# Kernel tuning notes

Measured on AMD Instinct MI355X. Metric: run time of the kernel, lower is better.

The kernel has to match this reference:

```python
import jax, jax.numpy as jnp
import numpy as np

VAL = 1.0  # shift weight value

def shift_plus(x, val=VAL):
    """Per-channel-group spatial shift ('+' mode), equivalent to the
    groups=C 3x3 conv with a single nonzero tap per channel, padding=1.
    x: [B, C, H, W], C % 5 == 0.
    """
    c = x.shape[1]
    cgp = c // 5
    xp = jnp.pad(x, ((0, 0), (0, 0), (1, 1), (1, 1)))
    g0 = xp[:, 0 * cgp:1 * cgp, 1:-1, 2:]    # tap (1,2): pull from w+1
    g1 = xp[:, 1 * cgp:2 * cgp, 1:-1, :-2]   # tap (1,0): pull from w-1
    g2 = xp[:, 2 * cgp:3 * cgp, 2:, 1:-1]    # tap (2,1): pull from h+1
    g3 = xp[:, 3 * cgp:4 * cgp, :-2, 1:-1]   # tap (0,1): pull from h-1
    g4 = x[:, 4 * cgp:, :, :]                # tap (1,1): identity
    return jnp.concatenate([g0, g1, g2, g3, g4], axis=1) * val

def shift_conv1x1(x, w, b):
    # shift then pointwise conv (1x1) with bias
    xs = shift_plus(x)
    y = jnp.einsum('bchw,oc->bohw', xs, w)
    return y + b[None, :, None, None]

def setup_inputs() -> dict:
    key = jax.random.key(0)
    k1, k2, k3, k4, k5 = jax.random.split(key, 5)
    B, Cin, H, W = 8, 100, 256, 256
    Chid, Cout = 200, 100
    x = jax.random.normal(k1, (B, Cin, H, W), dtype=jnp.float32)
    w1 = jax.random.normal(k2, (Chid, Cin), dtype=jnp.float32) * 0.02
    b1 = jax.random.normal(k3, (Chid,), dtype=jnp.float32) * 0.02
    w2 = jax.random.normal(k4, (Cout, Chid), dtype=jnp.float32) * 0.02
    b2 = jax.random.normal(k5, (Cout,), dtype=jnp.float32) * 0.02
    return {"x": x, "w1": w1, "b1": b1, "w2": w2, "b2": b2}

def reference(x, w1, b1, w2, b2):
    h = shift_conv1x1(x, w1, b1)
    h = jax.nn.gelu(h, approximate=False)  # torch nn.GELU default is exact erf
    return shift_conv1x1(h, w2, b2)
```

## Files before the change

### kernel.cpp

```cpp
#include <hip/hip_runtime.h>
#include <math.h>

typedef unsigned short u16;
typedef unsigned int   u32;
typedef short bf16x8 __attribute__((ext_vector_type(8)));
typedef float f32x4  __attribute__((ext_vector_type(4)));

__device__ __forceinline__ u16 f2bf(float f) {
  u32 u = __builtin_bit_cast(u32, f);
  u32 r = (u + 0x7fffu + ((u >> 16) & 1u)) >> 16;
  return (u16)r;
}
__device__ __forceinline__ float gelu_exact(float v) {
  return 0.5f * v * (1.0f + erff(v * 0.70710678118654752f));
}

#define H_BYTES   209715200ll
#define FW1_ELEMS 26624
#define FW2_ELEMS 25088

__global__ void prep_frags(const float* __restrict__ w1, const float* __restrict__ w2,
                           u16* __restrict__ fw1, u16* __restrict__ fw2) {
  int gid = blockIdx.x * 256 + threadIdx.x;
  if (gid < FW1_ELEMS) {
    int j = gid & 7, lane = (gid >> 3) & 63, rest = gid >> 9;
    int nt = rest % 13, kc = rest / 13;
    int c = kc * 32 + (lane >> 4) * 8 + j;
    int o = nt * 16 + (lane & 15);
    float v = (c < 100 && o < 200) ? w1[o * 100 + c] : 0.f;
    fw1[gid] = f2bf(v);
  } else if (gid < FW1_ELEMS + FW2_ELEMS) {
    int i2 = gid - FW1_ELEMS;
    int j = i2 & 7, lane = (i2 >> 3) & 63, rest = i2 >> 9;
    int nt = rest % 7, kc = rest / 7;
    int c = kc * 32 + (lane >> 4) * 8 + j;
    int o = nt * 16 + (lane & 15);
    float v = (c < 200 && o < 100) ? w2[o * 200 + c] : 0.f;
    fw2[i2] = f2bf(v);
  }
}

#define SK1  136
#define SKO1 208
__global__ __launch_bounds__(256, 3) void conv1_kernel(
    const float* __restrict__ x, const u16* __restrict__ fw1,
    const float* __restrict__ b1, u16* __restrict__ hbuf) {
  __shared__ __align__(16) char smem[128 * SKO1 * 2];
  u16* At = (u16*)smem;
  u16* Ot = (u16*)smem;
  const int t   = threadIdx.x;
  const int bid = blockIdx.x;
  const int bx  = ((bid & 7) << 9) | (bid >> 3);
  const int r  = bx >> 1;
  const int b  = r >> 8;
  const int hh = r & 255;
  const int w0 = (bx & 1) << 7;

  {
    const int m  = t & 127;
    const int kh = t >> 7;
    const int wp = w0 + m;
    #pragma unroll
    for (int g = 0; g < 8; ++g) {
      const int c0 = 8 * (kh + 2 * g);
      u32 pk[4];
      #pragma unroll
      for (int jj = 0; jj < 8; ++jj) {
        const int c = c0 + jj;
        float v = 0.f;
        if (c < 100) {
          const int dw = (c < 20) ? 1 : ((c < 40) ? -1 : 0);
          const int dh = (c >= 40 && c < 60) ? 1 : ((c >= 60 && c < 80) ? -1 : 0);
          const int hs = hh + dh, ws = wp + dw;
          if ((unsigned)hs < 256u && (unsigned)ws < 256u)
            v = x[((b * 100 + c) * 256 + hs) * 256 + ws];
        }
        const u32 bv = f2bf(v);
        if (jj & 1) pk[jj >> 1] |= bv << 16; else pk[jj >> 1] = bv;
      }
      *(uint4*)&At[m * SK1 + c0] = make_uint4(pk[0], pk[1], pk[2], pk[3]);
    }
  }
  __syncthreads();

  const int lane = t & 63, wid = t >> 6;
  const int col = lane & 15, q = lane >> 4;
  f32x4 acc[2][13];
  #pragma unroll
  for (int i = 0; i < 2; ++i)
    #pragma unroll
    for (int nt = 0; nt < 13; ++nt) acc[i][nt] = (f32x4)0.0f;

  const bf16x8* wf = (const bf16x8*)fw1 + lane;
  #pragma unroll 1
  for (int kc = 0; kc < 4; ++kc) {
    const bf16x8 a0 = *(const bf16x8*)&At[((2 * wid + 0) * 16 + col) * SK1 + kc * 32 + q * 8];
    const bf16x8 a1 = *(const bf16x8*)&At[((2 * wid + 1) * 16 + col) * SK1 + kc * 32 + q * 8];
    #pragma unroll
    for (int nt = 0; nt < 13; ++nt) {
      const bf16x8 bf = wf[(kc * 13 + nt) * 64];
      acc[0][nt] = __builtin_amdgcn_mfma_f32_16x16x32_bf16(bf, a0, acc[0][nt], 0, 0, 0);
      acc[1][nt] = __builtin_amdgcn_mfma_f32_16x16x32_bf16(bf, a1, acc[1][nt], 0, 0, 0);
    }
  }

  __syncthreads();

  #pragma unroll
  for (int nt = 0; nt < 13; ++nt) {
    const int ob = nt * 16 + 4 * q;
    const float4 bias4 = (ob <= 196) ? *(const float4*)&b1[ob]
                                     : make_float4(0.f, 0.f, 0.f, 0.f);
    #pragma unroll
    for (int i = 0; i < 2; ++i) {
      const f32x4 v = acc[i][nt];
      const int px = (2 * wid + i) * 16 + col;
      const u32 p0 = (u32)f2bf(gelu_exact(v[0] + bias4.x)) |
                     ((u32)f2bf(gelu_exact(v[1] + bias4.y)) << 16);
      const u32 p1 = (u32)f2bf(gelu_exact(v[2] + bias4.z)) |
                     ((u32)f2bf(gelu_exact(v[3] + bias4.w)) << 16);
      *(uint2*)&Ot[px * SKO1 + ob] = make_uint2(p0, p1);
    }
  }
  __syncthreads();
  {
    const int rowbase = ((b * 256 + hh) * 256 + w0) * 200;
    #pragma unroll
    for (int s = 0; s < 13; ++s) {
      const int id = s * 256 + t;
      if (id < 3200) {
        const int px = id / 25;
        const int ch = id - px * 25;
        const uint4 d = *(const uint4*)&Ot[px * SKO1 + ch * 8];
        *(uint4*)&hbuf[rowbase + px * 200 + ch * 8] = d;
      }
    }
  }
}

#define SK2 232
#define PS2 132
__global__ __launch_bounds__(256, 2) void conv2_kernel(
    const u16* __restrict__ hbuf, const u16* __restrict__ fw2,
    const float* __restrict__ b2, float* __restrict__ out) {
  __shared__ __align__(16) char smem[128 * SK2 * 2];
  u16*   At = (u16*)smem;
  float* Ob = (float*)smem;
  const int t   = threadIdx.x;
  const int bid = blockIdx.x;
  const int bx  = ((bid & 7) << 9) | (bid >> 3);
  const int r  = bx >> 1;
  const int b  = r >> 8;
  const int hh = r & 255;
  const int w0 = (bx & 1) << 7;

  {
    const int m  = t & 127;
    const int kh = t >> 7;
    const int wp = w0 + m;
    if (kh == 0) {
      const uint4 z = make_uint4(0u, 0u, 0u, 0u);
      *(uint4*)&At[m * SK2 + 200] = z;
      *(uint4*)&At[m * SK2 + 208] = z;
      *(uint4*)&At[m * SK2 + 216] = z;
    }
    #pragma unroll
    for (int g = 0; g < 13; ++g) {
      const int c0 = 8 * (kh + 2 * g);
      if (c0 < 200) {
        const int dw = (c0 < 40) ? 1 : ((c0 < 80) ? -1 : 0);
        const int dh = (c0 >= 80 && c0 < 120) ? 1 : ((c0 >= 120 && c0 < 160) ? -1 : 0);
        const int hs = hh + dh, ws = wp + dw;
        const bool ok = ((unsigned)hs < 256u) && ((unsigned)ws < 256u);
        const int hsc = ok ? hs : hh;
        const int wsc = ok ? ws : wp;
        uint4 d = *(const uint4*)&hbuf[((b * 256 + hsc) * 256 + wsc) * 200 + c0];
        if (!ok) d = make_uint4(0u, 0u, 0u, 0u);
        *(uint4*)&At[m * SK2 + c0] = d;
      }
    }
  }
  __syncthreads();

  const int lane = t & 63, wid = t >> 6;
  const int col = lane & 15, q = lane >> 4;
  f32x4 acc[2][7];
  #pragma unroll
  for (int i = 0; i < 2; ++i)
    #pragma unroll
    for (int nt = 0; nt < 7; ++nt) acc[i][nt] = (f32x4)0.0f;

  const bf16x8* wf = (const bf16x8*)fw2 + lane;
  #pragma unroll 1
  for (int kc = 0; kc < 7; ++kc) {
    const bf16x8 a0 = *(const bf16x8*)&At[((2 * wid + 0) * 16 + col) * SK2 + kc * 32 + q * 8];
    const bf16x8 a1 = *(const bf16x8*)&At[((2 * wid + 1) * 16 + col) * SK2 + kc * 32 + q * 8];
    #pragma unroll
    for (int nt = 0; nt < 7; ++nt) {
      const bf16x8 bf = wf[(kc * 7 + nt) * 64];
      acc[0][nt] = __builtin_amdgcn_mfma_f32_16x16x32_bf16(a0, bf, acc[0][nt], 0, 0, 0);
      acc[1][nt] = __builtin_amdgcn_mfma_f32_16x16x32_bf16(a1, bf, acc[1][nt], 0, 0, 0);
    }
  }

  __syncthreads();

  #pragma unroll
  for (int nt = 0; nt < 7; ++nt) {
    const int o = nt * 16 + col;
    const float bias = (o < 100) ? b2[o] : 0.f;
    #pragma unroll
    for (int i = 0; i < 2; ++i) {
      const f32x4 v = acc[i][nt];
      *(float4*)&Ob[o * PS2 + (2 * wid + i) * 16 + 4 * q] =
          make_float4(v[0] + bias, v[1] + bias, v[2] + bias, v[3] + bias);
    }
  }
  __syncthreads();
  {
    const int obase = (b * 100 * 256 + hh) * 256 + w0;
    #pragma unroll
    for (int s = 0; s < 13; ++s) {
      const int id = s * 256 + t;
      if (id < 3200) {
        const int oo = id >> 5, ch = id & 31;
        const float4 d = *(const float4*)&Ob[oo * PS2 + ch * 4];
        *(float4*)&out[obase + oo * 65536 + ch * 4] = d;
      }
    }
  }
}

extern "C" void kernel_launch(void* const* d_in, const int* in_sizes, int n_in,
                              void* d_out, int out_size, void* d_ws, size_t ws_size,
                              hipStream_t stream) {
  const float* x  = (const float*)d_in[0];
  const float* w1 = (const float*)d_in[1];
  const float* b1 = (const float*)d_in[2];
  const float* w2 = (const float*)d_in[3];
  const float* b2 = (const float*)d_in[4];
  float* out = (float*)d_out;

  u16* hbuf = (u16*)d_ws;
  u16* fw1  = (u16*)((char*)d_ws + H_BYTES);
  u16* fw2  = (u16*)((char*)d_ws + H_BYTES + FW1_ELEMS * 2);

  prep_frags<<<202, 256, 0, stream>>>(w1, w2, fw1, fw2);
  conv1_kernel<<<4096, 256, 0, stream>>>(x, fw1, b1, hbuf);
  conv2_kernel<<<4096, 256, 0, stream>>>(hbuf, fw2, b2, out);
}
```

Before: 608.2 us.

## Halve pixel tile per block to 64 and raise occupancy in both conv kernels

Both conv kernels now process 64 pixels per block instead of 128, and the grid doubles to 8192 blocks. Each wave handles one 16-pixel M-tile, which halves the accumulator registers and shared memory per block, and launch bounds rise to 4 blocks per SM. The goal is more waves in flight to hide global-memory latency in these bandwidth-bound kernels. In exchange, each weight fragment loaded from global or cache is reused across fewer pixels, and the row writes from each block become shorter.

```diff
diff --git a/kernel.cpp b/kernel.cpp
--- a/kernel.cpp
+++ b/kernel.cpp
@@ -42,27 +42,30 @@
 
 #define SK1  136
 #define SKO1 208
-__global__ __launch_bounds__(256, 3) void conv1_kernel(
+__global__ __launch_bounds__(256, 4) void conv1_kernel(
     const float* __restrict__ x, const u16* __restrict__ fw1,
     const float* __restrict__ b1, u16* __restrict__ hbuf) {
-  __shared__ __align__(16) char smem[128 * SKO1 * 2];
+  __shared__ __align__(16) char smem[64 * SKO1 * 2];
   u16* At = (u16*)smem;
   u16* Ot = (u16*)smem;
   const int t   = threadIdx.x;
   const int bid = blockIdx.x;
-  const int bx  = ((bid & 7) << 9) | (bid >> 3);
-  const int r  = bx >> 1;
-  const int b  = r >> 8;
-  const int hh = r & 255;
-  const int w0 = (bx & 1) << 7;
-
-  {
-    const int m  = t & 127;
-    const int kh = t >> 7;
+  const int bx  = ((bid & 7) << 10) | (bid >> 3);
+  const int b  = bx >> 10;
+  const int hh = (bx >> 2) & 255;
+  const int w0 = (bx & 3) << 6;
+
+  {
+    const int m  = t & 63;
+    const int kh = t >> 6;
     const int wp = w0 + m;
     #pragma unroll
-    for (int g = 0; g < 8; ++g) {
-      const int c0 = 8 * (kh + 2 * g);
+    for (int g = 0; g < 4; ++g) {
+      const int c0 = 8 * (kh + 4 * g);
+      if (c0 >= 100) {
+        *(uint4*)&At[m * SK1 + c0] = make_uint4(0u, 0u, 0u, 0u);
+        continue;
+      }
       u32 pk[4];
       #pragma unroll
       for (int jj = 0; jj < 8; ++jj) {
@@ -85,22 +88,18 @@
 
   const int lane = t & 63, wid = t >> 6;
   const int col = lane & 15, q = lane >> 4;
-  f32x4 acc[2][13];
-  #pragma unroll
-  for (int i = 0; i < 2; ++i)
-    #pragma unroll
-    for (int nt = 0; nt < 13; ++nt) acc[i][nt] = (f32x4)0.0f;
+  f32x4 acc[13];
+  #pragma unroll
+  for (int nt = 0; nt < 13; ++nt) acc[nt] = (f32x4)0.0f;
 
   const bf16x8* wf = (const bf16x8*)fw1 + lane;
   #pragma unroll 1
   for (int kc = 0; kc < 4; ++kc) {
-    const bf16x8 a0 = *(const bf16x8*)&At[((2 * wid + 0) * 16 + col) * SK1 + kc * 32 + q * 8];
-    const bf16x8 a1 = *(const bf16x8*)&At[((2 * wid + 1) * 16 + col) * SK1 + kc * 32 + q * 8];
+    const bf16x8 a = *(const bf16x8*)&At[(wid * 16 + col) * SK1 + kc * 32 + q * 8];
     #pragma unroll
     for (int nt = 0; nt < 13; ++nt) {
       const bf16x8 bf = wf[(kc * 13 + nt) * 64];
-      acc[0][nt] = __builtin_amdgcn_mfma_f32_16x16x32_bf16(bf, a0, acc[0][nt], 0, 0, 0);
-      acc[1][nt] = __builtin_amdgcn_mfma_f32_16x16x32_bf16(bf, a1, acc[1][nt], 0, 0, 0);
+      acc[nt] = __builtin_amdgcn_mfma_f32_16x16x32_bf16(bf, a, acc[nt], 0, 0, 0);
     }
   }
 
@@ -111,24 +110,21 @@
     const int ob = nt * 16 + 4 * q;
     const float4 bias4 = (ob <= 196) ? *(const float4*)&b1[ob]
                                      : make_float4(0.f, 0.f, 0.f, 0.f);
-    #pragma unroll
-    for (int i = 0; i < 2; ++i) {
-      const f32x4 v = acc[i][nt];
-      const int px = (2 * wid + i) * 16 + col;
-      const u32 p0 = (u32)f2bf(gelu_exact(v[0] + bias4.x)) |
-                     ((u32)f2bf(gelu_exact(v[1] + bias4.y)) << 16);
-      const u32 p1 = (u32)f2bf(gelu_exact(v[2] + bias4.z)) |
-                     ((u32)f2bf(gelu_exact(v[3] + bias4.w)) << 16);
-      *(uint2*)&Ot[px * SKO1 + ob] = make_uint2(p0, p1);
-    }
+    const f32x4 v = acc[nt];
+    const int px = wid * 16 + col;
+    const u32 p0 = (u32)f2bf(gelu_exact(v[0] + bias4.x)) |
+                   ((u32)f2bf(gelu_exact(v[1] + bias4.y)) << 16);
+    const u32 p1 = (u32)f2bf(gelu_exact(v[2] + bias4.z)) |
+                   ((u32)f2bf(gelu_exact(v[3] + bias4.w)) << 16);
+    *(uint2*)&Ot[px * SKO1 + ob] = make_uint2(p0, p1);
   }
   __syncthreads();
   {
     const int rowbase = ((b * 256 + hh) * 256 + w0) * 200;
     #pragma unroll
-    for (int s = 0; s < 13; ++s) {
+    for (int s = 0; s < 7; ++s) {
       const int id = s * 256 + t;
-      if (id < 3200) {
+      if (id < 1600) {
         const int px = id / 25;
         const int ch = id - px * 25;
         const uint4 d = *(const uint4*)&Ot[px * SKO1 + ch * 8];
@@ -139,67 +135,58 @@
 }
 
 #define SK2 232
-#define PS2 132
-__global__ __launch_bounds__(256, 2) void conv2_kernel(
+#define PS2 68
+__global__ __launch_bounds__(256, 4) void conv2_kernel(
     const u16* __restrict__ hbuf, const u16* __restrict__ fw2,
     const float* __restrict__ b2, float* __restrict__ out) {
-  __shared__ __align__(16) char smem[128 * SK2 * 2];
+  __shared__ __align__(16) char smem[112 * PS2 * 4];
   u16*   At = (u16*)smem;
   float* Ob = (float*)smem;
   const int t   = threadIdx.x;
   const int bid = blockIdx.x;
-  const int bx  = ((bid & 7) << 9) | (bid >> 3);
-  const int r  = bx >> 1;
-  const int b  = r >> 8;
-  const int hh = r & 255;
-  const int w0 = (bx & 1) << 7;
-
-  {
-    const int m  = t & 127;
-    const int kh = t >> 7;
+  const int bx  = ((bid & 7) << 10) | (bid >> 3);
+  const int b  = bx >> 10;
+  const int hh = (bx >> 2) & 255;
+  const int w0 = (bx & 3) << 6;
+
+  {
+    const int m  = t & 63;
+    const int kh = t >> 6;
     const int wp = w0 + m;
-    if (kh == 0) {
-      const uint4 z = make_uint4(0u, 0u, 0u, 0u);
-      *(uint4*)&At[m * SK2 + 200] = z;
-      *(uint4*)&At[m * SK2 + 208] = z;
-      *(uint4*)&At[m * SK2 + 216] = z;
-    }
-    #pragma unroll
-    for (int g = 0; g < 13; ++g) {
-      const int c0 = 8 * (kh + 2 * g);
-      if (c0 < 200) {
-        const int dw = (c0 < 40) ? 1 : ((c0 < 80) ? -1 : 0);
-        const int dh = (c0 >= 80 && c0 < 120) ? 1 : ((c0 >= 120 && c0 < 160) ? -1 : 0);
-        const int hs = hh + dh, ws = wp + dw;
-        const bool ok = ((unsigned)hs < 256u) && ((unsigned)ws < 256u);
-        const int hsc = ok ? hs : hh;
-        const int wsc = ok ? ws : wp;
-        uint4 d = *(const uint4*)&hbuf[((b * 256 + hsc) * 256 + wsc) * 200 + c0];
-        if (!ok) d = make_uint4(0u, 0u, 0u, 0u);
-        *(uint4*)&At[m * SK2 + c0] = d;
-      }
+    #pragma unroll
+    for (int g = 0; g < 7; ++g) {
+      const int c0 = 8 * (kh + 4 * g);
+      if (c0 >= 200) {
+        *(uint4*)&At[m * SK2 + c0] = make_uint4(0u, 0u, 0u, 0u);
+        continue;
+      }
+      const int dw = (c0 < 40) ? 1 : ((c0 < 80) ? -1 : 0);
+      const int dh = (c0 >= 80 && c0 < 120) ? 1 : ((c0 >= 120 && c0 < 160) ? -1 : 0);
+      const int hs = hh + dh, ws = wp + dw;
+      const bool ok = ((unsigned)hs < 256u) && ((unsigned)ws < 256u);
+      const int hsc = ok ? hs : hh;
+      const int wsc = ok ? ws : wp;
+      uint4 d = *(const uint4*)&hbuf[((b * 256 + hsc) * 256 + wsc) * 200 + c0];
+      if (!ok) d = make_uint4(0u, 0u, 0u, 0u);
+      *(uint4*)&At[m * SK2 + c0] = d;
     }
   }
   __syncthreads();
 
   const int lane = t & 63, wid = t >> 6;
   const int col = lane & 15, q = lane >> 4;
-  f32x4 acc[2][7];
-  #pragma unroll
-  for (int i = 0; i < 2; ++i)
-    #pragma unroll
-    for (int nt = 0; nt < 7; ++nt) acc[i][nt] = (f32x4)0.0f;
+  f32x4 acc[7];
+  #pragma unroll
+  for (int nt = 0; nt < 7; ++nt) acc[nt] = (f32x4)0.0f;
 
   const bf16x8* wf = (const bf16x8*)fw2 + lane;
   #pragma unroll 1
   for (int kc = 0; kc < 7; ++kc) {
-    const bf16x8 a0 = *(const bf16x8*)&At[((2 * wid + 0) * 16 + col) * SK2 + kc * 32 + q * 8];
-    const bf16x8 a1 = *(const bf16x8*)&At[((2 * wid + 1) * 16 + col) * SK2 + kc * 32 + q * 8];
+    const bf16x8 a = *(const bf16x8*)&At[(wid * 16 + col) * SK2 + kc * 32 + q * 8];
     #pragma unroll
     for (int nt = 0; nt < 7; ++nt) {
       const bf16x8 bf = wf[(kc * 7 + nt) * 64];
-      acc[0][nt] = __builtin_amdgcn_mfma_f32_16x16x32_bf16(a0, bf, acc[0][nt], 0, 0, 0);
-      acc[1][nt] = __builtin_amdgcn_mfma_f32_16x16x32_bf16(a1, bf, acc[1][nt], 0, 0, 0);
+      acc[nt] = __builtin_amdgcn_mfma_f32_16x16x32_bf16(a, bf, acc[nt], 0, 0, 0);
     }
   }
 
@@ -209,21 +196,18 @@
   for (int nt = 0; nt < 7; ++nt) {
     const int o = nt * 16 + col;
     const float bias = (o < 100) ? b2[o] : 0.f;
-    #pragma unroll
-    for (int i = 0; i < 2; ++i) {
-      const f32x4 v = acc[i][nt];
-      *(float4*)&Ob[o * PS2 + (2 * wid + i) * 16 + 4 * q] =
-          make_float4(v[0] + bias, v[1] + bias, v[2] + bias, v[3] + bias);
-    }
-  }
-  __syncthreads();
-  {
-    const int obase = (b * 100 * 256 + hh) * 256 + w0;
-    #pragma unroll
-    for (int s = 0; s < 13; ++s) {
+    const f32x4 v = acc[nt];
+    *(float4*)&Ob[o * PS2 + wid * 16 + 4 * q] =
+        make_float4(v[0] + bias, v[1] + bias, v[2] + bias, v[3] + bias);
+  }
+  __syncthreads();
+  {
+    const int obase = b * 6553600 + hh * 256 + w0;
+    #pragma unroll
+    for (int s = 0; s < 7; ++s) {
       const int id = s * 256 + t;
-      if (id < 3200) {
-        const int oo = id >> 5, ch = id & 31;
+      if (id < 1600) {
+        const int oo = id >> 4, ch = id & 15;
         const float4 d = *(const float4*)&Ob[oo * PS2 + ch * 4];
         *(float4*)&out[obase + oo * 65536 + ch * 4] = d;
       }
@@ -246,6 +230,6 @@
   u16* fw2  = (u16*)((char*)d_ws + H_BYTES + FW1_ELEMS * 2);
 
   prep_frags<<<202, 256, 0, stream>>>(w1, w2, fw1, fw2);
-  conv1_kernel<<<4096, 256, 0, stream>>>(x, fw1, b1, hbuf);
-  conv2_kernel<<<4096, 256, 0, stream>>>(hbuf, fw2, b2, out);
-}
+  conv1_kernel<<<8192, 256, 0, stream>>>(x, fw1, b1, hbuf);
+  conv2_kernel<<<8192, 256, 0, stream>>>(hbuf, fw2, b2, out);
+}
```

Measured after the change: 576.3 us. -5.2%, faster.
